# Optimization experiments

Hardware: AMD Instinct MI355X
Metric: run time of the kernel (lower is better)

## Reference

```python
import jax, jax.numpy as jnp
import numpy as np

N = 50000
E = 800000
D_IN = 256
H1 = 512   # hidden_channels
H2 = 256   # out_channels == hidden_dim
NUM_CLASSES = 5
NEG_SLOPE = 0.2


def _edge_softmax(logits, dst, n):
    # numerically-stable softmax over edges grouped by destination node
    m = jax.ops.segment_max(logits, dst, num_segments=n)
    e = jnp.exp(logits - m[dst])
    s = jax.ops.segment_sum(e, dst, num_segments=n)
    return e / (s[dst] + 1e-16)


def _gat_conv(x, src, dst, W, att_src, att_dst, bias):
    h = x @ W                                   # [N, C] (PyG lin_src, no bias)
    a_s = (h * att_src).sum(-1)                 # [N]
    a_d = (h * att_dst).sum(-1)                 # [N]
    logits = jax.nn.leaky_relu(a_s[src] + a_d[dst], NEG_SLOPE)  # [E]
    alpha = _edge_softmax(logits, dst, x.shape[0])              # [E]
    out = jax.ops.segment_sum(h[src] * alpha[:, None], dst, num_segments=x.shape[0])
    return out + bias


def setup_inputs() -> dict:
    key = jax.random.key(0)
    ks = jax.random.split(key, 20)
    g = lambda k, shp, fan: jax.random.normal(k, shp, jnp.float32) * (1.0 / np.sqrt(fan))
    inp = {
        "x": jax.random.normal(ks[0], (N, D_IN), jnp.float32),
        "edge_index": jax.random.randint(ks[1], (2, E), 0, N, jnp.int64),
        # conv1 (GATConv, heads=1)
        "W1": g(ks[2], (D_IN, H1), D_IN),
        "att_src1": g(ks[3], (H1,), H1),
        "att_dst1": g(ks[4], (H1,), H1),
        "b_conv1": jnp.zeros((H1,), jnp.float32),
        # lin1 (dense residual)
        "A1": g(ks[5], (D_IN, H1), D_IN),
        "b1": jnp.zeros((H1,), jnp.float32),
        # conv2
        "W2": g(ks[6], (H1, H2), H1),
        "att_src2": g(ks[7], (H2,), H2),
        "att_dst2": g(ks[8], (H2,), H2),
        "b_conv2": jnp.zeros((H2,), jnp.float32),
        # lin2
        "A2": g(ks[9], (H1, H2), H1),
        "b2": jnp.zeros((H2,), jnp.float32),
        # 3 hidden MLP layers [256 -> 256]
        "Hw1": g(ks[10], (H2, H2), H2), "Hb1": jnp.zeros((H2,), jnp.float32),
        "Hw2": g(ks[11], (H2, H2), H2), "Hb2": jnp.zeros((H2,), jnp.float32),
        "Hw3": g(ks[12], (H2, H2), H2), "Hb3": jnp.zeros((H2,), jnp.float32),
        # classifier
        "fcw": g(ks[13], (H2, NUM_CLASSES), H2),
        "fcb": jnp.zeros((NUM_CLASSES,), jnp.float32),
    }
    return inp


def reference(x, edge_index, W1, att_src1, att_dst1, b_conv1, A1, b1,
              W2, att_src2, att_dst2, b_conv2, A2, b2,
              Hw1, Hb1, Hw2, Hb2, Hw3, Hb3, fcw, fcb):
    src, dst = edge_index[0], edge_index[1]
    h = _gat_conv(x, src, dst, W1, att_src1, att_dst1, b_conv1) + (x @ A1 + b1)
    h = jax.nn.relu(h)
    h = _gat_conv(h, src, dst, W2, att_src2, att_dst2, b_conv2) + (h @ A2 + b2)
    for w, b in ((Hw1, Hb1), (Hw2, Hb2), (Hw3, Hb3)):
        h = jax.nn.relu(h @ w + b)
    logits = h @ fcw + fcb
    return jax.nn.softmax(logits, axis=-1)
```

## Files before the change

kernel.cpp:

```cpp
#include <hip/hip_runtime.h>

typedef unsigned short u16;
typedef short short8 __attribute__((ext_vector_type(8)));
typedef u16 u16x4 __attribute__((ext_vector_type(4)));
typedef u16 u16x8 __attribute__((ext_vector_type(8)));
typedef float float4v __attribute__((ext_vector_type(4)));

#define NEG_SLOPE 0.2f

static __device__ __forceinline__ float b2f(u16 u) {
    union { unsigned int i; float f; } x; x.i = ((unsigned int)u) << 16; return x.f;
}
static __device__ __forceinline__ u16 f2b(float f) {
    unsigned int u = __float_as_uint(f);
    unsigned int r = (u + 0x7fffu + ((u >> 16) & 1u)) >> 16;
    return (u16)r;
}

__global__ void k_diag(float* out, int n, float val)
{
    int i = blockIdx.x * 256 + threadIdx.x;
    if (i < n) out[i] = val;
}

__global__ void scan_csr(const int* off, const int* srcs, int N, int E,
                         int* flag, int bit)
{
    int i = blockIdx.x * 256 + threadIdx.x;
    if (i < N) {
        int a = off[i], b = off[i + 1];
        if (a < 0 || b < a || b > E) atomicOr(flag, bit);
    }
    if (i == 0 && off[N] != E) atomicOr(flag, bit);
    if (i < E) {
        if ((unsigned)srcs[i] >= (unsigned)N) atomicOr(flag, bit);
    }
}

__global__ void k_final_diag(const int* flag, float* out, int n)
{
    int f = *flag;
    if (f == 0) return;
    int b = __ffs(f) - 1;
    float val = 32.0f * (b + 1);
    int i = blockIdx.x * 256 + threadIdx.x;
    if (i < n) out[i] = val;
}

__global__ void k_detect(const int* ei, int E, int* flag64)
{
    __shared__ int zc;
    if (threadIdx.x == 0) zc = 0;
    __syncthreads();
    int idx = 1 + 2 * (int)threadIdx.x;
    int z = (idx < 2 * E && ei[idx] == 0) ? 1 : 0;
    atomicAdd(&zc, z);
    __syncthreads();
    if (threadIdx.x == 0) *flag64 = (zc >= 200) ? 1 : 0;
}

__global__ void k_extract(const int* ei, int E, const int* flag64,
                          int* src, int* dst, int* deg, int N)
{
    int e = blockIdx.x * 256 + threadIdx.x;
    if (e >= E) return;
    int s, d;
    if (*flag64) {
        s = ei[2 * e];
        d = ei[2 * E + 2 * e];
    } else {
        s = ei[e];
        d = ei[E + e];
    }
    src[e] = s; dst[e] = d;
    if ((unsigned)d < (unsigned)N) atomicAdd(&deg[d], 1);
}

__global__ __launch_bounds__(256)
void k_scan_a(const int* __restrict__ deg, int* __restrict__ off,
              int* __restrict__ partial, int N)
{
    __shared__ int sd[256];
    int tid = threadIdx.x;
    int base = blockIdx.x * 1024;
    int i0 = base + tid * 4;
    int v0 = 0, v1 = 0, v2 = 0, v3 = 0;
    if (i0 < N)     v0 = deg[i0];
    if (i0 + 1 < N) v1 = deg[i0 + 1];
    if (i0 + 2 < N) v2 = deg[i0 + 2];
    if (i0 + 3 < N) v3 = deg[i0 + 3];
    int t = v0 + v1 + v2 + v3;
    sd[tid] = t;
    __syncthreads();
    #pragma unroll
    for (int s = 1; s < 256; s <<= 1) {
        int u = (tid >= s) ? sd[tid - s] : 0;
        __syncthreads();
        sd[tid] += u;
        __syncthreads();
    }
    int excl = sd[tid] - t;
    if (i0 < N)     off[i0]     = excl;
    if (i0 + 1 < N) off[i0 + 1] = excl + v0;
    if (i0 + 2 < N) off[i0 + 2] = excl + v0 + v1;
    if (i0 + 3 < N) off[i0 + 3] = excl + v0 + v1 + v2;
    if (tid == 255) partial[blockIdx.x] = sd[255];
}

__global__ __launch_bounds__(1024)
void k_scan_b(int* partial, int nblk)
{
    __shared__ int sd[1024];
    __shared__ int running;
    int tid = threadIdx.x;
    if (tid == 0) running = 0;
    __syncthreads();
    for (int base = 0; base < nblk; base += 1024) {
        int i = base + tid;
        int v = (i < nblk) ? partial[i] : 0;
        sd[tid] = v;
        __syncthreads();
        for (int s = 1; s < 1024; s <<= 1) {
            int u = (tid >= s) ? sd[tid - s] : 0;
            __syncthreads();
            sd[tid] += u;
            __syncthreads();
        }
        if (i < nblk) partial[i] = sd[tid] - v + running;
        int total = sd[1023];
        __syncthreads();
        if (tid == 0) running += total;
        __syncthreads();
    }
}

__global__ __launch_bounds__(256)
void k_scan_c(int* __restrict__ off, int* __restrict__ cursor,
              const int* __restrict__ partial, int N, int E)
{
    int i = blockIdx.x * 256 + threadIdx.x;
    if (i < N) {
        int v = off[i] + partial[i >> 10];
        off[i] = v;
        cursor[i] = v;
    }
    if (i == 0) off[N] = E;
}

__global__ void k_scatter(const int* src, const int* dst, int* cursor,
                          int* srcs, int E, int N)
{
    int e = blockIdx.x * 256 + threadIdx.x;
    if (e < E) {
        int d = dst[e];
        if ((unsigned)d < (unsigned)N) {
            int p = atomicAdd(&cursor[d], 1);
            if ((unsigned)p < (unsigned)E) srcs[p] = src[e];
        }
    }
}

__global__ __launch_bounds__(256)
void k_castdot(const float* __restrict__ x, const float* __restrict__ vs,
               const float* __restrict__ vd, u16* __restrict__ xb,
               float* __restrict__ a_s, float* __restrict__ a_d, int N)
{
    int tid = threadIdx.x;
    int rowb = tid >> 5;
    int col8 = (tid & 31) * 8;
    int n = blockIdx.x * 8 + rowb;
    if (n >= N) return;
    const float* xr = x + (size_t)n * 256 + col8;
    float4 v0 = *(const float4*)xr;
    float4 v1 = *(const float4*)(xr + 4);
    int4 w;
    w.x = (int)f2b(v0.x) | ((int)f2b(v0.y) << 16);
    w.y = (int)f2b(v0.z) | ((int)f2b(v0.w) << 16);
    w.z = (int)f2b(v1.x) | ((int)f2b(v1.y) << 16);
    w.w = (int)f2b(v1.z) | ((int)f2b(v1.w) << 16);
    *(int4*)(xb + (size_t)n * 256 + col8) = w;

    float4 s0 = *(const float4*)(vs + col8);
    float4 s1 = *(const float4*)(vs + col8 + 4);
    float4 d0 = *(const float4*)(vd + col8);
    float4 d1 = *(const float4*)(vd + col8 + 4);
    float ss = v0.x*s0.x + v0.y*s0.y + v0.z*s0.z + v0.w*s0.w
             + v1.x*s1.x + v1.y*s1.y + v1.z*s1.z + v1.w*s1.w;
    float sd = v0.x*d0.x + v0.y*d0.y + v0.z*d0.z + v0.w*d0.w
             + v1.x*d1.x + v1.y*d1.y + v1.z*d1.z + v1.w*d1.w;
    #pragma unroll
    for (int m = 16; m; m >>= 1) {
        ss += __shfl_xor(ss, m, 64);
        sd += __shfl_xor(sd, m, 64);
    }
    if ((tid & 31) == 0) { a_s[n] = ss; a_d[n] = sd; }
}

__global__ __launch_bounds__(64)
void k_packAll(const float* A1w, const float* W1, const float* W2, const float* A2w,
               const float* Hw1, const float* Hw2, const float* Hw3,
               u16* WT1, u16* WT2, u16* WTH)
{
    int z = blockIdx.z;
    const float *in1, *in2; int ksplit, csplit, in_ld, NC16; u16* out;
    if (z == 0)      { in1 = A1w; in2 = W1;  ksplit = 256; csplit = 0;   in_ld = 512; out = WT1; NC16 = 32; }
    else if (z == 1) { in1 = W2;  in2 = A2w; ksplit = 0;   csplit = 256; in_ld = 256; out = WT2; NC16 = 32; }
    else {
        if (blockIdx.x >= 16 || blockIdx.y >= 8) return;
        in1 = (z == 2) ? Hw1 : (z == 3) ? Hw2 : Hw3;
        in2 = nullptr; ksplit = 0; csplit = 0; in_ld = 256; NC16 = 16;
        out = WTH + (size_t)(z - 2) * 65536;
    }
    int l = threadIdx.x;
    int cf = blockIdx.x, kt = blockIdx.y;
    int col = cf * 16 + (l & 15);
    int kbase = kt * 32 + (l >> 4) * 8;
    const float* src = in1;
    int cc = col, koff = 0;
    if (ksplit > 0 && kbase >= ksplit) { src = in2; koff = ksplit; }
    if (csplit > 0 && col >= csplit)   { src = in2; cc = col - csplit; }
    u16* o = out + ((size_t)(kt * NC16 + cf) * 512) + l * 8;
    #pragma unroll
    for (int j = 0; j < 8; ++j)
        o[j] = f2b(src[(size_t)(kbase - koff + j) * in_ld + cc]);
}

__global__ __launch_bounds__(256)
void k_rowdot2f(const float* __restrict__ A, int ld, int H,
                const float* __restrict__ vs, const float* __restrict__ vd,
                float* a_s, float* a_d, int N)
{
    int wave = threadIdx.x >> 6, lane = threadIdx.x & 63;
    int n = blockIdx.x * 4 + wave;
    if (n >= N) return;
    const float* ar = A + (size_t)n * ld;
    float ss = 0.f, sd = 0.f;
    for (int i = lane * 4; i < H; i += 256) {
        float4 v  = *(const float4*)(ar + i);
        float4 s4 = *(const float4*)(vs + i);
        float4 d4 = *(const float4*)(vd + i);
        ss += v.x * s4.x + v.y * s4.y + v.z * s4.z + v.w * s4.w;
        sd += v.x * d4.x + v.y * d4.y + v.z * d4.z + v.w * d4.w;
    }
    #pragma unroll
    for (int m = 32; m; m >>= 1) {
        ss += __shfl_xor(ss, m, 64);
        sd += __shfl_xor(sd, m, 64);
    }
    if (lane == 0) { a_s[n] = ss; a_d[n] = sd; }
}

__global__ __launch_bounds__(256)
void k_rowdot2(const u16* h, int ld, int H, const float* vs, const float* vd,
               float* a_s, float* a_d, int N)
{
    int wave = threadIdx.x >> 6, lane = threadIdx.x & 63;
    int n = blockIdx.x * 4 + wave;
    if (n >= N) return;
    const u16* hr = h + (size_t)n * ld;
    float ss = 0.f, sd = 0.f;
    for (int i = lane; i < H; i += 64) {
        float v = b2f(hr[i]);
        ss += v * vs[i];
        sd += v * vd[i];
    }
    #pragma unroll
    for (int m = 32; m; m >>= 1) {
        ss += __shfl_xor(ss, m, 64);
        sd += __shfl_xor(sd, m, 64);
    }
    if (lane == 0) { a_s[n] = ss; a_d[n] = sd; }
}

__global__ __launch_bounds__(256)
void k_alpha(const int* __restrict__ off, const int* __restrict__ srcs,
             const float* __restrict__ a_s, const float* __restrict__ a_d,
             float* __restrict__ alpha, int N)
{
    int wave = threadIdx.x >> 6, lane = threadIdx.x & 63;
    int n = blockIdx.x * 4 + wave;
    if (n >= N) return;
    int base = off[n], end = off[n + 1];
    float adn = a_d[n];
    float m = -1e30f, s = 0.f;
    for (int p = base + lane; p < end; p += 64) {
        int sx = srcs[p];
        sx = ((unsigned)sx < (unsigned)N) ? sx : 0;
        float z = a_s[sx] + adn;
        z = fmaxf(z, NEG_SLOPE * z);
        float mn = fmaxf(m, z);
        s = s * __expf(m - mn) + __expf(z - mn);
        m = mn;
    }
    #pragma unroll
    for (int msk = 32; msk; msk >>= 1) {
        float mo = __shfl_xor(m, msk, 64);
        float so = __shfl_xor(s, msk, 64);
        float mn = fmaxf(m, mo);
        s = s * __expf(m - mn) + so * __expf(mo - mn);
        m = mn;
    }
    float inv = 1.f / (s + 1e-16f);
    for (int p = base + lane; p < end; p += 64) {
        int sx = srcs[p];
        sx = ((unsigned)sx < (unsigned)N) ? sx : 0;
        float z = a_s[sx] + adn;
        z = fmaxf(z, NEG_SLOPE * z);
        alpha[p] = __expf(z - m) * inv;
    }
}

__global__ __launch_bounds__(256)
void k_aggw(const u16* __restrict__ rows, const int* __restrict__ off,
            const int* __restrict__ srcs, const float* __restrict__ alpha,
            const u16* __restrict__ add, u16* __restrict__ out, int N)
{
    int wave = threadIdx.x >> 6, lane = threadIdx.x & 63;
    int n = blockIdx.x * 4 + wave;
    if (n >= N) return;
    int base = off[n], end = off[n + 1];
    int half = lane >> 5;
    int c8 = (lane & 31) * 8;
    float acc[8] = {};
    int p = base;
    for (; p + 3 < end; p += 4) {
        int sA = srcs[p + half];
        int sB = srcs[p + 2 + half];
        sA = ((unsigned)sA < (unsigned)N) ? sA : 0;
        sB = ((unsigned)sB < (unsigned)N) ? sB : 0;
        float wA = alpha[p + half];
        float wB = alpha[p + 2 + half];
        u16x8 vA = *(const u16x8*)(rows + (size_t)sA * 256 + c8);
        u16x8 vB = *(const u16x8*)(rows + (size_t)sB * 256 + c8);
        #pragma unroll
        for (int j = 0; j < 8; ++j)
            acc[j] += wA * b2f(vA[j]) + wB * b2f(vB[j]);
    }
    for (; p + 1 < end; p += 2) {
        int sA = srcs[p + half];
        sA = ((unsigned)sA < (unsigned)N) ? sA : 0;
        float wA = alpha[p + half];
        u16x8 vA = *(const u16x8*)(rows + (size_t)sA * 256 + c8);
        #pragma unroll
        for (int j = 0; j < 8; ++j)
            acc[j] += wA * b2f(vA[j]);
    }
    if (p < end) {
        int sA = srcs[p];
        sA = ((unsigned)sA < (unsigned)N) ? sA : 0;
        float wA = half ? 0.f : alpha[p];
        u16x8 vA = *(const u16x8*)(rows + (size_t)sA * 256 + c8);
        #pragma unroll
        for (int j = 0; j < 8; ++j)
            acc[j] += wA * b2f(vA[j]);
    }
    #pragma unroll
    for (int j = 0; j < 8; ++j)
        acc[j] += __shfl_xor(acc[j], 32, 64);
    if (half == 0) {
        size_t ob = (size_t)n * 256 + c8;
        if (add) {
            u16x8 ad8 = *(const u16x8*)(add + ob);
            #pragma unroll
            for (int j = 0; j < 8; ++j) acc[j] += b2f(ad8[j]);
        }
        u16x8 o;
        #pragma unroll
        for (int j = 0; j < 8; ++j) o[j] = f2b(acc[j]);
        *(u16x8*)(out + ob) = o;
    }
}

__global__ __launch_bounds__(512)
void bigfull(const u16* __restrict__ A1, int lda1,
             const u16* __restrict__ A2, int lda2,
             const u16* __restrict__ WTf,
             const float* b0a, const float* b0b,
             const float* b1a, const float* b1b,
             u16* C1, int ldc1, u16* C2, int ldc2,
             int M, int relu0, int relu1)
{
    __shared__ u16 As[64 * 32];
    __shared__ u16 Bs[512 * 32];

    const int tid = threadIdx.x;
    const int w = tid >> 6, lane = tid & 63;
    const int m16 = lane & 15, q = lane >> 4;
    const int rowBase = blockIdx.x * 64;

    float4v acc[16] = {};

    for (int k0 = 0; k0 < 512; k0 += 32) {
        const int kt = k0 >> 5;
        __syncthreads();
        if (tid < 256) {
            int rf = tid >> 6, al = tid & 63;
            int grow = rowBase + rf * 16 + (al & 15);
            if (grow >= M) grow = M - 1;
            int kk = k0 + (al >> 4) * 8;
            const u16* src = (kk < 256)
                ? A1 + (size_t)grow * lda1 + kk
                : A2 + (size_t)grow * lda2 + (kk - 256);
            *(int4*)&As[tid * 8] = *(const int4*)src;
        }
        {
            const u16* wsrc = WTf + (size_t)kt * 16384;
            #pragma unroll
            for (int p = 0; p < 4; ++p) {
                int ch = p * 512 + tid;
                *(int4*)&Bs[ch * 8] = *(const int4*)(wsrc + (size_t)ch * 8);
            }
        }
        __syncthreads();

        short8 a[4], b[4];
        #pragma unroll
        for (int r = 0; r < 4; ++r)
            a[r] = *(const short8*)&As[r * 512 + lane * 8];
        #pragma unroll
        for (int c = 0; c < 4; ++c)
            b[c] = *(const short8*)&Bs[(w * 4 + c) * 512 + lane * 8];
        #pragma unroll
        for (int r = 0; r < 4; ++r)
            #pragma unroll
            for (int c = 0; c < 4; ++c)
                acc[r * 4 + c] = __builtin_amdgcn_mfma_f32_16x16x32_bf16(
                    a[r], b[c], acc[r * 4 + c], 0, 0, 0);
    }

    const int colgrp = w >> 2;
    const float* ba = colgrp ? b1a : b0a;
    const float* bb = colgrp ? b1b : b0b;
    u16* C  = colgrp ? C2 : C1;
    const int ldc  = colgrp ? ldc2 : ldc1;
    const int relu = colgrp ? relu1 : relu0;
    #pragma unroll
    for (int c = 0; c < 4; ++c) {
        int lc = ((w & 3) * 4 + c) * 16 + m16;
        float bv = (ba ? ba[lc] : 0.f) + (bb ? bb[lc] : 0.f);
        #pragma unroll
        for (int r = 0; r < 4; ++r)
            #pragma unroll
            for (int i = 0; i < 4; ++i) {
                int grow = rowBase + r * 16 + q * 4 + i;
                if (grow < M) {
                    float v = acc[r * 4 + c][i] + bv;
                    if (relu) v = fmaxf(v, 0.f);
                    C[(size_t)grow * ldc + lc] = f2b(v);
                }
            }
    }
}

__global__ __launch_bounds__(256)
void k_mlp3(const u16* __restrict__ WTHf,
            const float* Hb1, const float* Hb2, const float* Hb3,
            u16* H, int M)
{
    __shared__ u16 P[64 * 256];
    __shared__ u16 Bs[256 * 32];

    const int tid = threadIdx.x;
    const int w = tid >> 6, lane = tid & 63;
    const int m16 = lane & 15, q = lane >> 4;
    const int rowBase = blockIdx.x * 64;

    #pragma unroll
    for (int p = 0; p < 8; ++p) {
        int ch = p * 256 + tid;
        int f = ch >> 6, l = ch & 63;
        int kt = f >> 2, rf = f & 3;
        int grow = rowBase + rf * 16 + (l & 15);
        if (grow >= M) grow = M - 1;
        int col = kt * 32 + (l >> 4) * 8;
        *(int4*)&P[ch * 8] = *(const int4*)(H + (size_t)grow * 256 + col);
    }

    const float* biases[3] = {Hb1, Hb2, Hb3};
    for (int L = 0; L < 3; ++L) {
        const u16* WTf = WTHf + (size_t)L * 65536;
        float4v acc[16] = {};
        for (int kt = 0; kt < 8; ++kt) {
            __syncthreads();
            {
                const u16* wsrc = WTf + (size_t)kt * 8192;
                #pragma unroll
                for (int p = 0; p < 4; ++p) {
                    int ch = p * 256 + tid;
                    *(int4*)&Bs[ch * 8] = *(const int4*)(wsrc + (size_t)ch * 8);
                }
            }
            __syncthreads();
            short8 a[4], b[4];
            #pragma unroll
            for (int r = 0; r < 4; ++r)
                a[r] = *(const short8*)&P[(kt * 4 + r) * 512 + lane * 8];
            #pragma unroll
            for (int c = 0; c < 4; ++c)
                b[c] = *(const short8*)&Bs[(w * 4 + c) * 512 + lane * 8];
            #pragma unroll
            for (int r = 0; r < 4; ++r)
                #pragma unroll
                for (int c = 0; c < 4; ++c)
                    acc[r * 4 + c] = __builtin_amdgcn_mfma_f32_16x16x32_bf16(
                        a[r], b[c], acc[r * 4 + c], 0, 0, 0);
        }
        const float* bias = biases[L];
        __syncthreads();
        if (L < 2) {
            #pragma unroll
            for (int c = 0; c < 4; ++c) {
                int col = w * 64 + c * 16 + m16;
                float bv = bias[col];
                int kt2 = col >> 5;
                int l2h = 16 * ((col & 31) >> 3);
                int j2 = col & 7;
                #pragma unroll
                for (int r = 0; r < 4; ++r)
                    #pragma unroll
                    for (int i = 0; i < 4; ++i) {
                        int l2 = (q * 4 + i) + l2h;
                        P[(size_t)(kt2 * 4 + r) * 512 + l2 * 8 + j2] =
                            f2b(fmaxf(acc[r * 4 + c][i] + bv, 0.f));
                    }
            }
        } else {
            #pragma unroll
            for (int c = 0; c < 4; ++c) {
                int col = w * 64 + c * 16 + m16;
                float bv = bias[col];
                #pragma unroll
                for (int r = 0; r < 4; ++r)
                    #pragma unroll
                    for (int i = 0; i < 4; ++i) {
                        int grow = rowBase + r * 16 + q * 4 + i;
                        if (grow < M)
                            H[(size_t)grow * 256 + col] =
                                f2b(fmaxf(acc[r * 4 + c][i] + bv, 0.f));
                    }
            }
        }
    }
}

__global__ __launch_bounds__(256)
void k_fc_softmax(const u16* hin, const float* fcw, const float* fcb,
                  float* out, int N)
{
    int wave = threadIdx.x >> 6, lane = threadIdx.x & 63;
    int n = blockIdx.x * 4 + wave;
    if (n >= N) return;
    const u16* hr = hin + (size_t)n * 256;
    int k0 = lane * 4;
    float hv[4];
    float p[5] = {0.f, 0.f, 0.f, 0.f, 0.f};
    #pragma unroll
    for (int j = 0; j < 4; ++j) hv[j] = b2f(hr[k0 + j]);
    #pragma unroll
    for (int j = 0; j < 4; ++j) {
        const float* wr = fcw + (size_t)(k0 + j) * 5;
        #pragma unroll
        for (int c = 0; c < 5; ++c) p[c] += hv[j] * wr[c];
    }
    #pragma unroll
    for (int c = 0; c < 5; ++c) {
        #pragma unroll
        for (int s = 32; s; s >>= 1) p[c] += __shfl_xor(p[c], s, 64);
    }
    if (lane == 0) {
        float m = -1e30f;
        #pragma unroll
        for (int c = 0; c < 5; ++c) { p[c] += fcb[c]; m = fmaxf(m, p[c]); }
        float s = 0.f, e[5];
        #pragma unroll
        for (int c = 0; c < 5; ++c) { e[c] = __expf(p[c] - m); s += e[c]; }
        float inv = 1.f / s;
        #pragma unroll
        for (int c = 0; c < 5; ++c) out[(size_t)n * 5 + c] = e[c] * inv;
    }
}

extern "C" void kernel_launch(void* const* d_in, const int* in_sizes, int n_in,
                              void* d_out, int out_size, void* d_ws, size_t ws_size,
                              hipStream_t stream)
{
    const float* x    = (const float*)d_in[0];
    const int*   ei   = (const int*)  d_in[1];
    const float* W1   = (const float*)d_in[2];
    const float* as1  = (const float*)d_in[3];
    const float* ad1  = (const float*)d_in[4];
    const float* bc1  = (const float*)d_in[5];
    const float* A1w  = (const float*)d_in[6];
    const float* b1   = (const float*)d_in[7];
    const float* W2   = (const float*)d_in[8];
    const float* as2  = (const float*)d_in[9];
    const float* ad2  = (const float*)d_in[10];
    const float* bc2  = (const float*)d_in[11];
    const float* A2w  = (const float*)d_in[12];
    const float* b2   = (const float*)d_in[13];
    const float* Hw1  = (const float*)d_in[14];
    const float* Hb1  = (const float*)d_in[15];
    const float* Hw2  = (const float*)d_in[16];
    const float* Hb2  = (const float*)d_in[17];
    const float* Hw3  = (const float*)d_in[18];
    const float* Hb3  = (const float*)d_in[19];
    const float* fcw  = (const float*)d_in[20];
    const float* fcb  = (const float*)d_in[21];
    float* out = (float*)d_out;

    const int D = 256;
    const int N = in_sizes[0] / D;
    const int E = in_sizes[1] / 2;

    char* w = (char*)d_ws;
    auto alloc = [&](size_t bytes) {
        char* p = w;
        w += (bytes + 255) & ~(size_t)255;
        return p;
    };
    int*   flag   = (int*)  alloc(256);
    int*   flag64 = (int*)  alloc(256);
    float* a_s    = (float*)alloc((size_t)N * 4);
    float* a_d    = (float*)alloc((size_t)N * 4);
    float* vs1    = (float*)alloc(1024);
    float* vd1    = (float*)alloc(1024);
    int*   deg    = (int*)  alloc((size_t)N * 4);
    int*   cursor = (int*)  alloc((size_t)N * 4);
    int*   offA   = (int*)  alloc((size_t)(N + 1) * 4);
    int*   part   = (int*)  alloc((size_t)((N + 1023) / 1024 + 1) * 4);
    int*   srcs   = (int*)  alloc((size_t)E * 4);
    float* alpha  = (float*)alloc((size_t)E * 4);
    u16*   WT1    = (u16*)  alloc(512 * 512 * 2);
    u16*   WT2    = (u16*)  alloc(512 * 512 * 2);
    u16*   WTH    = (u16*)  alloc(3 * 256 * 256 * 2);
    u16*   BUF1   = (u16*)  alloc((size_t)N * 512 * 2);
    u16*   BUF2   = (u16*)  alloc((size_t)N * 512 * 2);

    int* src32 = (int*)BUF1;
    int* dst32 = src32 + E;

    size_t need = (size_t)(w - (char*)d_ws);
    if (ws_size < need) {
        float code = 1000.0f + (float)(ws_size >> 20);
        k_diag<<<(out_size + 255) / 256, 256, 0, stream>>>(out, out_size, code);
        return;
    }

    const int EB  = (E + 255) / 256;
    const int NB4 = (N + 3) / 4;
    const int OB  = (out_size + 255) / 256;
    const int NE  = (N > E ? N : E);
    const int RB64 = (N + 63) / 64;
    const int NBLK = (N + 1023) / 1024;
    const size_t NH2 = (size_t)N * 256;
    u16* XB   = BUF1;
    u16* AGGX = BUF1 + NH2;

    hipMemsetAsync(flag, 0, 4, stream);
    hipMemsetAsync(deg, 0, (size_t)N * 4, stream);

    k_detect <<<1, 256, 0, stream>>>(ei, E, flag64);
    k_extract<<<EB, 256, 0, stream>>>(ei, E, flag64, src32, dst32, deg, N);
    k_scan_a <<<NBLK, 256, 0, stream>>>(deg, offA, part, N);
    k_scan_b <<<1, 1024, 0, stream>>>(part, NBLK);
    k_scan_c <<<(N + 255) / 256, 256, 0, stream>>>(offA, cursor, part, N, E);
    k_scatter<<<EB, 256, 0, stream>>>(src32, dst32, cursor, srcs, E, N);
    scan_csr <<<(NE + 255) / 256, 256, 0, stream>>>(offA, srcs, N, E, flag, 1);

    k_packAll<<<dim3(32, 16, 5), 64, 0, stream>>>(A1w, W1, W2, A2w,
                                                  Hw1, Hw2, Hw3, WT1, WT2, WTH);

    k_rowdot2f<<<64, 256, 0, stream>>>(W1, 512, 512, as1, ad1, vs1, vd1, 256);
    k_castdot<<<(N + 7) / 8, 256, 0, stream>>>(x, vs1, vd1, XB, a_s, a_d, N);
    k_alpha<<<NB4, 256, 0, stream>>>(offA, srcs, a_s, a_d, alpha, N);

    k_aggw<<<NB4, 256, 0, stream>>>(XB, offA, srcs, alpha, nullptr, AGGX, N);

    bigfull<<<RB64, 512, 0, stream>>>(XB, 256, AGGX, 256, WT1,
                                      b1, bc1, b1 + 256, bc1 + 256,
                                      BUF2, 512, BUF2 + 256, 512, N, 1, 1);

    bigfull<<<RB64, 512, 0, stream>>>(BUF2, 512, BUF2 + 256, 512, WT2,
                                      nullptr, nullptr, b2, bc2,
                                      BUF1, 256, BUF1 + NH2, 256, N, 0, 0);

    k_rowdot2<<<NB4, 256, 0, stream>>>(BUF1, 256, 256, as2, ad2, a_s, a_d, N);
    k_alpha<<<NB4, 256, 0, stream>>>(offA, srcs, a_s, a_d, alpha, N);
    k_aggw<<<NB4, 256, 0, stream>>>(BUF1, offA, srcs, alpha, BUF1 + NH2, BUF2, N);

    k_mlp3<<<RB64, 256, 0, stream>>>(WTH, Hb1, Hb2, Hb3, BUF2, N);

    k_fc_softmax<<<NB4, 256, 0, stream>>>(BUF2, fcw, fcb, out, N);

    k_final_diag<<<OB, 256, 0, stream>>>(flag, out, out_size);
}
```

Baseline: 587.1 us.

## Load GEMM weight fragments straight from global and fuse FC softmax into MLP kernel

```diff
diff --git a/kernel.cpp b/kernel.cpp
--- a/kernel.cpp
+++ b/kernel.cpp
@@ -381,7 +381,6 @@
              int M, int relu0, int relu1)
 {
     __shared__ u16 As[64 * 32];
-    __shared__ u16 Bs[512 * 32];
 
     const int tid = threadIdx.x;
     const int w = tid >> 6, lane = tid & 63;
@@ -403,23 +402,18 @@
                 : A2 + (size_t)grow * lda2 + (kk - 256);
             *(int4*)&As[tid * 8] = *(const int4*)src;
         }
-        {
-            const u16* wsrc = WTf + (size_t)kt * 16384;
-            #pragma unroll
-            for (int p = 0; p < 4; ++p) {
-                int ch = p * 512 + tid;
-                *(int4*)&Bs[ch * 8] = *(const int4*)(wsrc + (size_t)ch * 8);
-            }
-        }
         __syncthreads();
 
         short8 a[4], b[4];
+        #pragma unroll
+        for (int c = 0; c < 4; ++c) {
+            int4 bv = *(const int4*)(WTf + (size_t)kt * 16384
+                                     + (size_t)(w * 4 + c) * 512 + lane * 8);
+            b[c] = *(short8*)&bv;
+        }
         #pragma unroll
         for (int r = 0; r < 4; ++r)
             a[r] = *(const short8*)&As[r * 512 + lane * 8];
-        #pragma unroll
-        for (int c = 0; c < 4; ++c)
-            b[c] = *(const short8*)&Bs[(w * 4 + c) * 512 + lane * 8];
         #pragma unroll
         for (int r = 0; r < 4; ++r)
             #pragma unroll
@@ -453,12 +447,12 @@
 }
 
 __global__ __launch_bounds__(256)
-void k_mlp3(const u16* __restrict__ WTHf,
-            const float* Hb1, const float* Hb2, const float* Hb3,
-            u16* H, int M)
+void k_mlp3fc(const u16* __restrict__ WTHf,
+              const float* Hb1, const float* Hb2, const float* Hb3,
+              const float* __restrict__ fcw, const float* __restrict__ fcb,
+              const u16* __restrict__ Hin, float* __restrict__ out, int M)
 {
     __shared__ u16 P[64 * 256];
-    __shared__ u16 Bs[256 * 32];
 
     const int tid = threadIdx.x;
     const int w = tid >> 6, lane = tid & 63;
@@ -473,31 +467,26 @@
         int grow = rowBase + rf * 16 + (l & 15);
         if (grow >= M) grow = M - 1;
         int col = kt * 32 + (l >> 4) * 8;
-        *(int4*)&P[ch * 8] = *(const int4*)(H + (size_t)grow * 256 + col);
-    }
+        *(int4*)&P[ch * 8] = *(const int4*)(Hin + (size_t)grow * 256 + col);
+    }
+    __syncthreads();
 
     const float* biases[3] = {Hb1, Hb2, Hb3};
     for (int L = 0; L < 3; ++L) {
         const u16* WTf = WTHf + (size_t)L * 65536;
         float4v acc[16] = {};
+        #pragma unroll 2
         for (int kt = 0; kt < 8; ++kt) {
-            __syncthreads();
-            {
-                const u16* wsrc = WTf + (size_t)kt * 8192;
-                #pragma unroll
-                for (int p = 0; p < 4; ++p) {
-                    int ch = p * 256 + tid;
-                    *(int4*)&Bs[ch * 8] = *(const int4*)(wsrc + (size_t)ch * 8);
-                }
+            short8 a[4], b[4];
+            #pragma unroll
+            for (int c = 0; c < 4; ++c) {
+                int4 bv = *(const int4*)(WTf + (size_t)(kt * 16 + w * 4 + c) * 512
+                                         + lane * 8);
+                b[c] = *(short8*)&bv;
             }
-            __syncthreads();
-            short8 a[4], b[4];
             #pragma unroll
             for (int r = 0; r < 4; ++r)
                 a[r] = *(const short8*)&P[(kt * 4 + r) * 512 + lane * 8];
-            #pragma unroll
-            for (int c = 0; c < 4; ++c)
-                b[c] = *(const short8*)&Bs[(w * 4 + c) * 512 + lane * 8];
             #pragma unroll
             for (int r = 0; r < 4; ++r)
                 #pragma unroll
@@ -507,76 +496,54 @@
         }
         const float* bias = biases[L];
         __syncthreads();
-        if (L < 2) {
-            #pragma unroll
-            for (int c = 0; c < 4; ++c) {
-                int col = w * 64 + c * 16 + m16;
-                float bv = bias[col];
-                int kt2 = col >> 5;
-                int l2h = 16 * ((col & 31) >> 3);
-                int j2 = col & 7;
+        #pragma unroll
+        for (int c = 0; c < 4; ++c) {
+            int col = w * 64 + c * 16 + m16;
+            float bv = bias[col];
+            int kt2 = col >> 5;
+            int l2h = 16 * ((col & 31) >> 3);
+            int j2 = col & 7;
+            #pragma unroll
+            for (int r = 0; r < 4; ++r)
                 #pragma unroll
-                for (int r = 0; r < 4; ++r)
-                    #pragma unroll
-                    for (int i = 0; i < 4; ++i) {
-                        int l2 = (q * 4 + i) + l2h;
-                        P[(size_t)(kt2 * 4 + r) * 512 + l2 * 8 + j2] =
-                            f2b(fmaxf(acc[r * 4 + c][i] + bv, 0.f));
-                    }
-            }
-        } else {
-            #pragma unroll
-            for (int c = 0; c < 4; ++c) {
-                int col = w * 64 + c * 16 + m16;
-                float bv = bias[col];
-                #pragma unroll
-                for (int r = 0; r < 4; ++r)
-                    #pragma unroll
-                    for (int i = 0; i < 4; ++i) {
-                        int grow = rowBase + r * 16 + q * 4 + i;
-                        if (grow < M)
-                            H[(size_t)grow * 256 + col] =
-                                f2b(fmaxf(acc[r * 4 + c][i] + bv, 0.f));
-                    }
-            }
-        }
-    }
-}
-
-__global__ __launch_bounds__(256)
-void k_fc_softmax(const u16* hin, const float* fcw, const float* fcb,
-                  float* out, int N)
-{
-    int wave = threadIdx.x >> 6, lane = threadIdx.x & 63;
-    int n = blockIdx.x * 4 + wave;
-    if (n >= N) return;
-    const u16* hr = hin + (size_t)n * 256;
-    int k0 = lane * 4;
-    float hv[4];
-    float p[5] = {0.f, 0.f, 0.f, 0.f, 0.f};
-    #pragma unroll
-    for (int j = 0; j < 4; ++j) hv[j] = b2f(hr[k0 + j]);
-    #pragma unroll
-    for (int j = 0; j < 4; ++j) {
-        const float* wr = fcw + (size_t)(k0 + j) * 5;
-        #pragma unroll
-        for (int c = 0; c < 5; ++c) p[c] += hv[j] * wr[c];
+                for (int i = 0; i < 4; ++i) {
+                    int l2 = (q * 4 + i) + l2h;
+                    P[(size_t)(kt2 * 4 + r) * 512 + l2 * 8 + j2] =
+                        f2b(fmaxf(acc[r * 4 + c][i] + bv, 0.f));
+                }
+        }
+        __syncthreads();
+    }
+
+    float p5[5] = {0.f, 0.f, 0.f, 0.f, 0.f};
+    #pragma unroll
+    for (int kt = 0; kt < 8; ++kt) {
+        u16x8 v = *(const u16x8*)&P[(kt * 4 + w) * 512 + lane * 8];
+        int colb = kt * 32 + q * 8;
+        #pragma unroll
+        for (int j = 0; j < 8; ++j) {
+            float hv = b2f(v[j]);
+            const float* wr = fcw + (size_t)(colb + j) * 5;
+            #pragma unroll
+            for (int c = 0; c < 5; ++c) p5[c] += hv * wr[c];
+        }
     }
     #pragma unroll
     for (int c = 0; c < 5; ++c) {
-        #pragma unroll
-        for (int s = 32; s; s >>= 1) p[c] += __shfl_xor(p[c], s, 64);
-    }
-    if (lane == 0) {
-        float m = -1e30f;
-        #pragma unroll
-        for (int c = 0; c < 5; ++c) { p[c] += fcb[c]; m = fmaxf(m, p[c]); }
+        p5[c] += __shfl_xor(p5[c], 16, 64);
+        p5[c] += __shfl_xor(p5[c], 32, 64);
+    }
+    int grow = rowBase + w * 16 + m16;
+    if (q == 0 && grow < M) {
+        float mx = -1e30f;
+        #pragma unroll
+        for (int c = 0; c < 5; ++c) { p5[c] += fcb[c]; mx = fmaxf(mx, p5[c]); }
         float s = 0.f, e[5];
         #pragma unroll
-        for (int c = 0; c < 5; ++c) { e[c] = __expf(p[c] - m); s += e[c]; }
+        for (int c = 0; c < 5; ++c) { e[c] = __expf(p5[c] - mx); s += e[c]; }
         float inv = 1.f / s;
         #pragma unroll
-        for (int c = 0; c < 5; ++c) out[(size_t)n * 5 + c] = e[c] * inv;
+        for (int c = 0; c < 5; ++c) out[(size_t)grow * 5 + c] = e[c] * inv;
     }
 }
 
@@ -688,9 +655,8 @@
     k_alpha<<<NB4, 256, 0, stream>>>(offA, srcs, a_s, a_d, alpha, N);
     k_aggw<<<NB4, 256, 0, stream>>>(BUF1, offA, srcs, alpha, BUF1 + NH2, BUF2, N);
 
-    k_mlp3<<<RB64, 256, 0, stream>>>(WTH, Hb1, Hb2, Hb3, BUF2, N);
-
-    k_fc_softmax<<<NB4, 256, 0, stream>>>(BUF2, fcw, fcb, out, N);
+    k_mlp3fc<<<RB64, 256, 0, stream>>>(WTH, Hb1, Hb2, Hb3, fcw, fcb,
+                                       BUF2, out, N);
 
     k_final_diag<<<OB, 256, 0, stream>>>(flag, out, out_size);
 }
```

Result: faster. 572.4 us (-2.5%).
